# Kernel optimization log

Hardware: AMD Instinct MI355X
Metric: run time of the kernel (lower is better)

## Reference

```python
import jax, jax.numpy as jnp
import numpy as np

B, S, D_IN, D_OUT = 8, 2048, 512, 512


def setup_inputs() -> dict:
    key = jax.random.key(0)
    ks = jax.random.split(key, 6)
    return {
        "inputs_for_keys": jax.random.normal(ks[0], (B, S, D_IN), dtype=jnp.float32),
        "inputs_for_values": jax.random.normal(ks[1], (B, S, D_IN), dtype=jnp.float32),
        "inputs_for_queries": jax.random.normal(ks[2], (B, S, D_IN), dtype=jnp.float32),
        "Wq": jax.random.normal(ks[3], (D_IN, D_OUT), dtype=jnp.float32) * 0.05,
        "Wk": jax.random.normal(ks[4], (D_IN, D_OUT), dtype=jnp.float32) * 0.05,
        "Wv": jax.random.normal(ks[5], (D_IN, D_OUT), dtype=jnp.float32) * 0.05,
    }


def reference(inputs_for_keys, inputs_for_values, inputs_for_queries, Wq, Wk, Wv):
    # Projections: [B,S,D_in] @ [D_in,D_out] -> [B,S,D_out]
    Q = inputs_for_queries @ Wq
    K = inputs_for_keys @ Wk
    V = inputs_for_values @ Wv
    d_k = K.shape[-1]
    scale = 1.0 / jnp.sqrt(jnp.float32(d_k))
    # Scores: [B,Sq,Sk]
    scores = jnp.einsum("bqd,bkd->bqk", Q, K) * scale
    # Causal mask: original adds -inf for key positions j > query i (use_mask=True)
    q_idx = jnp.arange(Q.shape[1])[:, None]
    k_idx = jnp.arange(K.shape[1])[None, :]
    scores = jnp.where(k_idx > q_idx, jnp.float32(-jnp.inf), scores)
    attn = jax.nn.softmax(scores, axis=-1)
    return jnp.einsum("bqk,bkd->bqd", attn, V)
```

## Files before the change

kernel.cpp:

```cpp
#include <hip/hip_runtime.h>
#include <hip/hip_bf16.h>

typedef __bf16 bf16;
typedef __bf16 bf16x4 __attribute__((ext_vector_type(4)));
typedef __bf16 bf16x8 __attribute__((ext_vector_type(8)));
typedef float f32x4 __attribute__((ext_vector_type(4)));
typedef float f32x16 __attribute__((ext_vector_type(16)));

#define NB 8
#define NS 2048
#define ND 512

static __device__ __forceinline__ f32x4 mfma16(bf16x8 a, bf16x8 b, f32x4 c) {
  return __builtin_amdgcn_mfma_f32_16x16x32_bf16(a, b, c, 0, 0, 0);
}
static __device__ __forceinline__ f32x16 mfma32(bf16x8 a, bf16x8 b, f32x16 c) {
  return __builtin_amdgcn_mfma_f32_32x32x16_bf16(a, b, c, 0, 0, 0);
}
static __device__ __forceinline__ void async16(const bf16* g, bf16* l) {
  __builtin_amdgcn_global_load_lds((const __attribute__((address_space(1))) void*)g,
                                   (__attribute__((address_space(3))) void*)l, 16, 0, 0);
}

#define BAR_VM8_LG0() do { asm volatile("s_waitcnt vmcnt(8) lgkmcnt(0)" ::: "memory"); \
  __builtin_amdgcn_s_barrier(); __builtin_amdgcn_sched_barrier(0); } while (0)
#define BAR_LG0() do { asm volatile("s_waitcnt lgkmcnt(0)" ::: "memory"); \
  __builtin_amdgcn_s_barrier(); __builtin_amdgcn_sched_barrier(0); } while (0)

__global__ void wconv_kernel(const float* __restrict__ Wq,
                             const float* __restrict__ Wk,
                             const float* __restrict__ Wv,
                             bf16* __restrict__ Wt) {
  __shared__ float buf[64][65];
  const int z = blockIdx.z;
  const float* W = (z == 0) ? Wq : (z == 1) ? Wk : Wv;
  const float scale = (z == 0) ? 0.063763537f : 1.0f;
  const int k0 = blockIdx.x * 64, n0 = blockIdx.y * 64;
  const int t = threadIdx.x;
#pragma unroll
  for (int i = 0; i < 16; ++i) {
    int idx = i * 256 + t;
    int kk = idx >> 6, nn = idx & 63;
    buf[kk][nn] = W[(size_t)(k0 + kk) * 512 + n0 + nn];
  }
  __syncthreads();
#pragma unroll
  for (int i = 0; i < 16; ++i) {
    int idx = i * 256 + t;
    int nn = idx >> 6, kk = idx & 63;
    Wt[(size_t)z * 262144 + (size_t)(n0 + nn) * 512 + k0 + kk] = (bf16)(buf[kk][nn] * scale);
  }
}

__launch_bounds__(256)
__global__ void proj_kernel(const float* __restrict__ Xq,
                            const float* __restrict__ Xk,
                            const float* __restrict__ Xv,
                            const bf16* __restrict__ Wt,
                            bf16* __restrict__ Cq,
                            bf16* __restrict__ Ck,
                            bf16* __restrict__ Cv) {
  __shared__ bf16 As[2][128][72];
  __shared__ bf16 Ws[2][128][72];
  const int z = blockIdx.z;
  const float* A = (z == 0) ? Xq : (z == 1) ? Xk : Xv;
  const bf16* Wz = Wt + (size_t)z * 262144;
  bf16* C = (z == 0) ? Cq : (z == 1) ? Ck : Cv;

  const int t = threadIdx.x;
  const int lane = t & 63;
  const int w = t >> 6;
  const int wr = w >> 1, wc = w & 1;
  const int bxr = blockIdx.x;
  const int mt = (bxr & 7) * 16 + (bxr >> 3);
  const int bm = mt * 128;
  const int bn = blockIdx.y * 128;

  f32x4 acc[4][4] = {};

  auto stageA = [&](int kc, int bufi) {
    int r0 = t >> 4, seg = t & 15;
#pragma unroll
    for (int p = 0; p < 8; ++p) {
      int r = p * 16 + r0;
      float4 v = *(const float4*)(A + (size_t)(bm + r) * 512 + kc * 64 + seg * 4);
      bf16x4 o = {(bf16)v.x, (bf16)v.y, (bf16)v.z, (bf16)v.w};
      *(bf16x4*)&As[bufi][r][seg * 4] = o;
    }
  };
  auto stageW = [&](int kc, int bufi) {
    int n0 = t >> 3, seg = t & 7;
#pragma unroll
    for (int p = 0; p < 4; ++p) {
      int n = p * 32 + n0;
      bf16x8 v = *(const bf16x8*)(Wz + (size_t)(bn + n) * 512 + kc * 64 + seg * 8);
      *(bf16x8*)&Ws[bufi][n][seg * 8] = v;
    }
  };

  stageA(0, 0);
  stageW(0, 0);
  __syncthreads();
  int buf = 0;
  for (int kc = 0; kc < 8; ++kc) {
    if (kc < 7) { stageA(kc + 1, buf ^ 1); stageW(kc + 1, buf ^ 1); }
    const int arow = lane & 15, kq = (lane >> 4) * 8;
#pragma unroll
    for (int kk = 0; kk < 2; ++kk) {
      bf16x8 af[4], bfr[4];
#pragma unroll
      for (int mi = 0; mi < 4; ++mi)
        af[mi] = *(const bf16x8*)&As[buf][wr * 64 + mi * 16 + arow][kk * 32 + kq];
#pragma unroll
      for (int ni = 0; ni < 4; ++ni)
        bfr[ni] = *(const bf16x8*)&Ws[buf][wc * 64 + ni * 16 + arow][kk * 32 + kq];
#pragma unroll
      for (int mi = 0; mi < 4; ++mi)
#pragma unroll
        for (int ni = 0; ni < 4; ++ni)
          acc[mi][ni] = mfma16(af[mi], bfr[ni], acc[mi][ni]);
    }
    __syncthreads();
    buf ^= 1;
  }

  const int row0 = (lane >> 4) * 4, col = lane & 15;
#pragma unroll
  for (int mi = 0; mi < 4; ++mi)
#pragma unroll
    for (int ni = 0; ni < 4; ++ni) {
      int cg = bn + wc * 64 + ni * 16 + col;
#pragma unroll
      for (int j = 0; j < 4; ++j) {
        int rg = bm + wr * 64 + mi * 16 + row0 + j;
        bf16 o = (bf16)acc[mi][ni][j];
        if (z == 0) {
          C[(size_t)rg * ND + cg] = o;
        } else if (z == 1) {
          C[(size_t)rg * ND + (cg ^ ((rg & 7) << 3))] = o;
        } else {
          int bb = rg >> 11, s = rg & 2047;
          int ss = (s & ~63) | ((s & 63) ^ ((cg & 7) << 3));
          C[(size_t)bb * (ND * NS) + (size_t)cg * NS + ss] = o;
        }
      }
    }
}

template<int NSPLIT>
__launch_bounds__(512, 2)
__global__ void attn_kernel(const bf16* __restrict__ Qg,
                            const bf16* __restrict__ Kg,
                            const bf16* __restrict__ Vtg,
                            float* __restrict__ Out,
                            bf16* __restrict__ Pn,
                            float* __restrict__ Mp,
                            float* __restrict__ Lp) {
  __shared__ bf16 Ks[64][512];
  __shared__ bf16 Vts[512][64];
  __shared__ float Ss[64][68];
  __shared__ bf16 Ps[64][72];
  __shared__ float m_lds[64], l_lds[64], r_lds[64];

  const int t = threadIdx.x;
  const int lane = t & 63;
  const int w = t >> 6;
  const int id = blockIdx.x;
  const int b = id & 7;
  const int qt = 31 - ((id >> 3) & 31);
  const int h = (NSPLIT == 2) ? (id >> 8) : 0;
  const int q0 = qt * 64;
  const int sm = w >> 1, sn = w & 1;
  const int l15 = lane & 15, lq = lane >> 4;
  const int l31 = lane & 31, lhi = lane >> 5;

  int t_begin, t_end;
  {
    int nt = qt + 1;
    int mid = (nt + 1) >> 1;
    if (NSPLIT == 2) { t_begin = h ? mid : 0; t_end = h ? nt : mid; }
    else { t_begin = 0; t_end = nt; }
  }
  const int pidx = (h * 8 + b) * 32 + qt;

  if (NSPLIT == 2 && t_begin >= t_end) {
    if (t < 64) { Mp[pidx * 64 + t] = -1e30f; Lp[pidx * 64 + t] = 0.0f; }
    return;
  }

  const bf16* Qb = Qg + (size_t)b * NS * ND;
  const bf16* Kb = Kg + (size_t)b * NS * ND;
  const bf16* Vb = Vtg + (size_t)b * ND * NS;

  if (t < 64) { m_lds[t] = -1e30f; l_lds[t] = 0.0f; }

  bf16x8 qf[16];
  {
    const bf16* qrow = Qb + (size_t)(q0 + sm * 16 + l15) * ND + lq * 8;
#pragma unroll
    for (int kc = 0; kc < 16; ++kc) qf[kc] = *(const bf16x8*)(qrow + kc * 32);
  }
  f32x16 acc[2][2] = {};

  auto stageK = [&](int k0s) {
#pragma unroll
    for (int i = 0; i < 8; ++i)
      async16(Kb + (size_t)(k0s + w * 8 + i) * ND + lane * 8, &Ks[w * 8 + i][0]);
  };
  auto stageV = [&](int k0s) {
#pragma unroll
    for (int i = 0; i < 8; ++i)
      async16(Vb + (size_t)(w * 64 + i * 8 + (lane >> 3)) * NS + k0s + (lane & 7) * 8,
              &Vts[w * 64 + i * 8][0]);
  };

  stageK(t_begin * 64);
  stageV(t_begin * 64);

  for (int it = t_begin; it < t_end; ++it) {
    const int k0 = it * 64;
    const int nx = (it + 1 < t_end ? it + 1 : it) * 64;
    BAR_VM8_LG0();

    f32x4 s0 = {}, s1 = {};
    const int kr0 = sn * 32 + l15, kr1 = kr0 + 16;
    const int swz = (l15 & 7) << 3;
#pragma unroll
    for (int kc = 0; kc < 16; ++kc) {
      const int colb = (kc * 32 + lq * 8) ^ swz;
      bf16x8 b0 = *(const bf16x8*)&Ks[kr0][colb];
      bf16x8 b1 = *(const bf16x8*)&Ks[kr1][colb];
      s0 = mfma16(qf[kc], b0, s0);
      s1 = mfma16(qf[kc], b1, s1);
    }
    {
      const bool mask = (it == qt);
#pragma unroll
      for (int j = 0; j < 4; ++j) {
        const int qr = sm * 16 + lq * 4 + j;
        float v0 = s0[j], v1 = s1[j];
        if (mask) {
          if (k0 + kr0 > q0 + qr) v0 = -1e30f;
          if (k0 + kr1 > q0 + qr) v1 = -1e30f;
        }
        Ss[qr][kr0] = v0;
        Ss[qr][kr1] = v1;
      }
    }
    BAR_LG0();
    stageK(nx);

    {
      const int row = t >> 3, sub = t & 7;
      float4 a = *(const float4*)&Ss[row][sub * 8];
      float4 c = *(const float4*)&Ss[row][sub * 8 + 4];
      float mx = fmaxf(fmaxf(fmaxf(a.x, a.y), fmaxf(a.z, a.w)),
                       fmaxf(fmaxf(c.x, c.y), fmaxf(c.z, c.w)));
#pragma unroll
      for (int d = 1; d < 8; d <<= 1) mx = fmaxf(mx, __shfl_xor(mx, d));
      float m_old = m_lds[row];
      float m_new = fmaxf(m_old, mx);
      float p0 = exp2f(a.x - m_new), p1 = exp2f(a.y - m_new);
      float p2 = exp2f(a.z - m_new), p3 = exp2f(a.w - m_new);
      float p4 = exp2f(c.x - m_new), p5 = exp2f(c.y - m_new);
      float p6 = exp2f(c.z - m_new), p7 = exp2f(c.w - m_new);
      float sum = ((p0 + p1) + (p2 + p3)) + ((p4 + p5) + (p6 + p7));
#pragma unroll
      for (int d = 1; d < 8; d <<= 1) sum += __shfl_xor(sum, d);
      bf16x8 pv = {(bf16)p0, (bf16)p1, (bf16)p2, (bf16)p3,
                   (bf16)p4, (bf16)p5, (bf16)p6, (bf16)p7};
      *(bf16x8*)&Ps[row][sub * 8] = pv;
      if (sub == 0) {
        float rs = exp2f(m_old - m_new);
        r_lds[row] = rs;
        m_lds[row] = m_new;
        l_lds[row] = l_lds[row] * rs + sum;
      }
    }
    BAR_VM8_LG0();

#pragma unroll
    for (int mi = 0; mi < 2; ++mi)
#pragma unroll
      for (int j = 0; j < 16; ++j) {
        int row = mi * 32 + (j & 3) + 8 * (j >> 2) + 4 * lhi;
        float rs = r_lds[row];
        acc[mi][0][j] *= rs;
        acc[mi][1][j] *= rs;
      }
#pragma unroll
    for (int kc = 0; kc < 4; ++kc) {
      const int kv0 = kc * 16 + lhi * 8;
      bf16x8 pa0 = *(const bf16x8*)&Ps[l31][kv0];
      bf16x8 pa1 = *(const bf16x8*)&Ps[32 + l31][kv0];
      bf16x8 vb0, vb1;
      { int d0 = w * 64 + l31;      vb0 = *(const bf16x8*)&Vts[d0][kv0 ^ ((d0 & 7) << 3)]; }
      { int d1 = w * 64 + 32 + l31; vb1 = *(const bf16x8*)&Vts[d1][kv0 ^ ((d1 & 7) << 3)]; }
      acc[0][0] = mfma32(pa0, vb0, acc[0][0]);
      acc[0][1] = mfma32(pa0, vb1, acc[0][1]);
      acc[1][0] = mfma32(pa1, vb0, acc[1][0]);
      acc[1][1] = mfma32(pa1, vb1, acc[1][1]);
    }
    BAR_LG0();
    stageV(nx);
  }

  if (NSPLIT == 2) {
    if (t < 64) { Mp[pidx * 64 + t] = m_lds[t]; Lp[pidx * 64 + t] = l_lds[t]; }
    bf16* Ob = Pn + (size_t)pidx * 64 * ND;
#pragma unroll
    for (int mi = 0; mi < 2; ++mi)
#pragma unroll
      for (int j = 0; j < 16; ++j) {
        int row = mi * 32 + (j & 3) + 8 * (j >> 2) + 4 * lhi;
        float inv = 1.0f / l_lds[row];
#pragma unroll
        for (int ni = 0; ni < 2; ++ni)
          Ob[(size_t)row * ND + w * 64 + ni * 32 + l31] = (bf16)(acc[mi][ni][j] * inv);
      }
  } else {
    float* Ob = Out + (size_t)b * NS * ND;
#pragma unroll
    for (int mi = 0; mi < 2; ++mi)
#pragma unroll
      for (int j = 0; j < 16; ++j) {
        int row = mi * 32 + (j & 3) + 8 * (j >> 2) + 4 * lhi;
        float inv = 1.0f / l_lds[row];
#pragma unroll
        for (int ni = 0; ni < 2; ++ni)
          __builtin_nontemporal_store(acc[mi][ni][j] * inv,
              &Ob[(size_t)(q0 + row) * ND + w * 64 + ni * 32 + l31]);
      }
  }
}

__global__ void combine_kernel(const bf16* __restrict__ Pn,
                               const float* __restrict__ Mp,
                               const float* __restrict__ Lp,
                               float* __restrict__ Out) {
  const int total = NB * NS * ND / 4;
  for (int v = blockIdx.x * 256 + threadIdx.x; v < total; v += gridDim.x * 256) {
    int e = v * 4;
    int d = e & 511;
    int s = (e >> 9) & 2047;
    int bb = e >> 20;
    int qt = s >> 6, r = s & 63;
    int p0 = (bb * 32 + qt) * 64 + r;
    int p1 = ((8 + bb) * 32 + qt) * 64 + r;
    float m0 = Mp[p0], l0 = Lp[p0], m1 = Mp[p1], l1 = Lp[p1];
    float M = fmaxf(m0, m1);
    float w0 = l0 * exp2f(m0 - M), w1 = l1 * exp2f(m1 - M);
    float inv = 1.0f / (w0 + w1);
    bf16x4 o0 = *(const bf16x4*)(Pn + (size_t)p0 * ND + d);
    bf16x4 o1 = *(const bf16x4*)(Pn + (size_t)p1 * ND + d);
    f32x4 o;
    o[0] = (w0 * (float)o0[0] + w1 * (float)o1[0]) * inv;
    o[1] = (w0 * (float)o0[1] + w1 * (float)o1[1]) * inv;
    o[2] = (w0 * (float)o0[2] + w1 * (float)o1[2]) * inv;
    o[3] = (w0 * (float)o0[3] + w1 * (float)o1[3]) * inv;
    __builtin_nontemporal_store(o, (f32x4*)(Out + e));
  }
}

extern "C" void kernel_launch(void* const* d_in, const int* in_sizes, int n_in,
                              void* d_out, int out_size, void* d_ws, size_t ws_size,
                              hipStream_t stream) {
  const float* Xk = (const float*)d_in[0];
  const float* Xv = (const float*)d_in[1];
  const float* Xq = (const float*)d_in[2];
  const float* Wq = (const float*)d_in[3];
  const float* Wk = (const float*)d_in[4];
  const float* Wv = (const float*)d_in[5];
  float* Out = (float*)d_out;

  char* ws = (char*)d_ws;
  bf16* Qb = (bf16*)(ws);
  bf16* Kb = (bf16*)(ws + (size_t)16 * 1024 * 1024);
  bf16* Vt = (bf16*)(ws + (size_t)32 * 1024 * 1024);
  bf16* Wt = (bf16*)(ws + (size_t)48 * 1024 * 1024);
  bf16* Pn = (bf16*)(ws + (size_t)50 * 1024 * 1024);
  float* Mp = (float*)(ws + (size_t)82 * 1024 * 1024);
  float* Lp = (float*)(ws + (size_t)82 * 1024 * 1024 + 131072);
  const bool split = ws_size >= (size_t)83 * 1024 * 1024;

  wconv_kernel<<<dim3(8, 8, 3), 256, 0, stream>>>(Wq, Wk, Wv, Wt);
  proj_kernel<<<dim3(128, 4, 3), 256, 0, stream>>>(Xq, Xk, Xv, Wt, Qb, Kb, Vt);
  if (split) {
    attn_kernel<2><<<512, 512, 0, stream>>>(Qb, Kb, Vt, Out, Pn, Mp, Lp);
    combine_kernel<<<2048, 256, 0, stream>>>(Pn, Mp, Lp, Out);
  } else {
    attn_kernel<1><<<256, 512, 0, stream>>>(Qb, Kb, Vt, Out, Pn, Mp, Lp);
  }
}
```

Before: 162.7 us.

## Split QK^T over head dim with 32x32 MFMA, async swizzled W staging

In the projection GEMM, the transposed weights are stored pre-swizzled and loaded into LDS with async global-to-LDS copies instead of register round-trips, and reads apply the XOR swizzle. In attention, the QK^T step now uses 32x32x16 MFMAs with warps split across the 512-wide head dimension. One half writes partial scores to LDS and the other half adds them and applies the mask, which costs an extra barrier. s_setprio is raised around the MFMA sections to favour matrix issue.

```diff
diff --git a/kernel.cpp b/kernel.cpp
--- a/kernel.cpp
+++ b/kernel.cpp
@@ -48,7 +48,8 @@
   for (int i = 0; i < 16; ++i) {
     int idx = i * 256 + t;
     int nn = idx >> 6, kk = idx & 63;
-    Wt[(size_t)z * 262144 + (size_t)(n0 + nn) * 512 + k0 + kk] = (bf16)(buf[kk][nn] * scale);
+    Wt[(size_t)z * 262144 + (size_t)(n0 + nn) * 512 + k0 + (kk ^ ((nn & 7) << 3))] =
+        (bf16)(buf[kk][nn] * scale);
   }
 }
 
@@ -61,7 +62,7 @@
                             bf16* __restrict__ Ck,
                             bf16* __restrict__ Cv) {
   __shared__ bf16 As[2][128][72];
-  __shared__ bf16 Ws[2][128][72];
+  __shared__ bf16 WsL[2][8192];
   const int z = blockIdx.z;
   const float* A = (z == 0) ? Xq : (z == 1) ? Xk : Xv;
   const bf16* Wz = Wt + (size_t)z * 262144;
@@ -89,21 +90,19 @@
     }
   };
   auto stageW = [&](int kc, int bufi) {
-    int n0 = t >> 3, seg = t & 7;
-#pragma unroll
-    for (int p = 0; p < 4; ++p) {
-      int n = p * 32 + n0;
-      bf16x8 v = *(const bf16x8*)(Wz + (size_t)(bn + n) * 512 + kc * 64 + seg * 8);
-      *(bf16x8*)&Ws[bufi][n][seg * 8] = v;
-    }
+    const int n = t >> 3, seg = t & 7;
+#pragma unroll
+    for (int i = 0; i < 4; ++i)
+      async16(Wz + (size_t)(bn + i * 32 + n) * 512 + kc * 64 + seg * 8,
+              &WsL[bufi][(i * 32 + n) * 64 + seg * 8]);
   };
 
+  stageW(0, 0);
   stageA(0, 0);
-  stageW(0, 0);
   __syncthreads();
   int buf = 0;
   for (int kc = 0; kc < 8; ++kc) {
-    if (kc < 7) { stageA(kc + 1, buf ^ 1); stageW(kc + 1, buf ^ 1); }
+    if (kc < 7) { stageW(kc + 1, buf ^ 1); stageA(kc + 1, buf ^ 1); }
     const int arow = lane & 15, kq = (lane >> 4) * 8;
 #pragma unroll
     for (int kk = 0; kk < 2; ++kk) {
@@ -112,8 +111,10 @@
       for (int mi = 0; mi < 4; ++mi)
         af[mi] = *(const bf16x8*)&As[buf][wr * 64 + mi * 16 + arow][kk * 32 + kq];
 #pragma unroll
-      for (int ni = 0; ni < 4; ++ni)
-        bfr[ni] = *(const bf16x8*)&Ws[buf][wc * 64 + ni * 16 + arow][kk * 32 + kq];
+      for (int ni = 0; ni < 4; ++ni) {
+        int n = wc * 64 + ni * 16 + arow;
+        bfr[ni] = *(const bf16x8*)&WsL[buf][n * 64 + ((kk * 32 + kq) ^ ((n & 7) << 3))];
+      }
 #pragma unroll
       for (int mi = 0; mi < 4; ++mi)
 #pragma unroll
@@ -170,8 +171,7 @@
   const int qt = 31 - ((id >> 3) & 31);
   const int h = (NSPLIT == 2) ? (id >> 8) : 0;
   const int q0 = qt * 64;
-  const int sm = w >> 1, sn = w & 1;
-  const int l15 = lane & 15, lq = lane >> 4;
+  const int sm = w >> 2, sn = (w >> 1) & 1, sk = w & 1;
   const int l31 = lane & 31, lhi = lane >> 5;
 
   int t_begin, t_end;
@@ -196,9 +196,9 @@
 
   bf16x8 qf[16];
   {
-    const bf16* qrow = Qb + (size_t)(q0 + sm * 16 + l15) * ND + lq * 8;
-#pragma unroll
-    for (int kc = 0; kc < 16; ++kc) qf[kc] = *(const bf16x8*)(qrow + kc * 32);
+    const bf16* qrow = Qb + (size_t)(q0 + sm * 32 + l31) * ND + sk * 256 + lhi * 8;
+#pragma unroll
+    for (int kc = 0; kc < 16; ++kc) qf[kc] = *(const bf16x8*)(qrow + kc * 16);
   }
   f32x16 acc[2][2] = {};
 
@@ -222,33 +222,38 @@
     const int nx = (it + 1 < t_end ? it + 1 : it) * 64;
     BAR_VM8_LG0();
 
-    f32x4 s0 = {}, s1 = {};
-    const int kr0 = sn * 32 + l15, kr1 = kr0 + 16;
-    const int swz = (l15 & 7) << 3;
+    __builtin_amdgcn_s_setprio(1);
+    f32x16 sacc = {};
+    const int kvr = sn * 32 + l31;
+    const int swz = (kvr & 7) << 3;
 #pragma unroll
     for (int kc = 0; kc < 16; ++kc) {
-      const int colb = (kc * 32 + lq * 8) ^ swz;
-      bf16x8 b0 = *(const bf16x8*)&Ks[kr0][colb];
-      bf16x8 b1 = *(const bf16x8*)&Ks[kr1][colb];
-      s0 = mfma16(qf[kc], b0, s0);
-      s1 = mfma16(qf[kc], b1, s1);
-    }
-    {
-      const bool mask = (it == qt);
-#pragma unroll
-      for (int j = 0; j < 4; ++j) {
-        const int qr = sm * 16 + lq * 4 + j;
-        float v0 = s0[j], v1 = s1[j];
-        if (mask) {
-          if (k0 + kr0 > q0 + qr) v0 = -1e30f;
-          if (k0 + kr1 > q0 + qr) v1 = -1e30f;
-        }
-        Ss[qr][kr0] = v0;
-        Ss[qr][kr1] = v1;
+      int col = (sk * 256 + kc * 16 + lhi * 8) ^ swz;
+      bf16x8 bfrag = *(const bf16x8*)&Ks[kvr][col];
+      sacc = mfma32(qf[kc], bfrag, sacc);
+    }
+    __builtin_amdgcn_s_setprio(0);
+    if (sk) {
+#pragma unroll
+      for (int j = 0; j < 16; ++j) {
+        int row = (j & 3) + 8 * (j >> 2) + 4 * lhi;
+        Ss[sm * 32 + row][sn * 32 + l31] = sacc[j];
       }
     }
     BAR_LG0();
     stageK(nx);
+    if (!sk) {
+      const bool mask = (it == qt);
+#pragma unroll
+      for (int j = 0; j < 16; ++j) {
+        int row = (j & 3) + 8 * (j >> 2) + 4 * lhi;
+        int q = sm * 32 + row, kvc = sn * 32 + l31;
+        float v = sacc[j] + Ss[q][kvc];
+        if (mask && (k0 + kvc > q0 + q)) v = -1e30f;
+        Ss[q][kvc] = v;
+      }
+    }
+    BAR_LG0();
 
     {
       const int row = t >> 3, sub = t & 7;
@@ -279,6 +284,7 @@
     }
     BAR_VM8_LG0();
 
+    __builtin_amdgcn_s_setprio(1);
 #pragma unroll
     for (int mi = 0; mi < 2; ++mi)
 #pragma unroll
@@ -301,6 +307,7 @@
       acc[1][0] = mfma32(pa1, vb0, acc[1][0]);
       acc[1][1] = mfma32(pa1, vb1, acc[1][1]);
     }
+    __builtin_amdgcn_s_setprio(0);
     BAR_LG0();
     stageV(nx);
   }
```

Measured after the change: 165.3 us. Within noise of the previous version (+1.6%).
